# Optimization experiments

Hardware: AMD Instinct MI355X
Metric: run time of the kernel (lower is better)

Reference implementation:

```python
import jax, jax.numpy as jnp
import numpy as np

SR = 16000.0
WIN = 400
SHIFT = 160
NMEL = 80
PREEMPH = 0.97
EPS = float(np.finfo(np.float64).eps)


def _mel_banks(num_bins, win, sr):
    # kaldi-compatible triangular mel banks, low_freq=20, high_freq=nyquist
    def hz2mel(f):
        return 1127.0 * np.log(1.0 + f / 700.0)
    mlow, mhigh = hz2mel(20.0), hz2mel(sr / 2.0)
    d = (mhigh - mlow) / (num_bins + 1)
    left = mlow + np.arange(num_bins) * d
    center = left + d
    right = left + 2 * d
    fft_freqs = (sr / win) * np.arange(win // 2)
    mel = hz2mel(fft_freqs)[None, :]
    up = (mel - left[:, None]) / d
    down = (right[:, None] - mel) / d
    banks = np.maximum(0.0, np.minimum(up, down))
    banks = np.concatenate([banks, np.zeros((num_bins, 1))], axis=1)  # pad last rfft bin
    return jnp.asarray(banks, jnp.float32)

_BANKS = _mel_banks(NMEL, WIN, SR)
_WINDOW = jnp.asarray(0.5 - 0.5 * np.cos(2 * np.pi * np.arange(WIN) / (WIN - 1)), jnp.float32)


def setup_inputs() -> dict:
    key = jax.random.key(0)
    k1, k2 = jax.random.split(key)
    B, L = 64, 240000
    x = jax.random.normal(k1, (B, L), dtype=jnp.float32)
    T = jax.random.randint(k2, (B,), 1, L, dtype=jnp.int32)
    normalizer = jnp.full((NMEL,), 0.1, dtype=jnp.float32)  # Parameter init 1/10
    return {"x": x, "T": T, "normalizer": normalizer}


def _fbank(x, normalizer):
    B, L = x.shape
    n_frames = 1 + (L - WIN) // SHIFT  # snip_edges=True
    idx = np.arange(n_frames)[:, None] * SHIFT + np.arange(WIN)[None, :]
    frames = x[:, idx]
    # preemphasis: frame[i] -= 0.97 * frame[i-1]; first sample uses itself
    prev = jnp.concatenate([frames[..., :1], frames[..., :-1]], axis=-1)
    frames = (frames - PREEMPH * prev) * _WINDOW
    spec = jnp.abs(jnp.fft.rfft(frames, axis=-1)) ** 2
    mel = jnp.einsum('bfk,mk->bfm', spec, _BANKS)
    mel = jnp.log(jnp.maximum(mel, EPS))
    return mel * normalizer[None, None, :]


def reference(x, T, normalizer):
    fb = _fbank(x, normalizer)                            # (B, F, M)
    B, F, M = fb.shape
    # faithful to source: downsample_factor = max(T) / fbanks[0].shape[1] (= num_mel_bins)
    ds = jnp.max(T).astype(jnp.float32) / M
    T_ = (T.astype(jnp.float32) / ds).astype(jnp.int32)   # int() truncation, T >= 0
    mask = (jnp.arange(F)[None, :] < T_[:, None])[..., None]  # (B, F, 1)
    cnt = jnp.maximum(T_, 1).astype(fb.dtype)[:, None, None]
    mean = jnp.sum(jnp.where(mask, fb, 0.0), axis=1, keepdims=True) / cnt
    return jnp.where(mask, fb - mean, fb)
```

## Files before the change

kernel.cpp:

```cpp
#include <hip/hip_runtime.h>
#include <hip/hip_bf16.h>

#define BATCH   64
#define LSIG    240000
#define WIN     400
#define SHIFT   160
#define NFR     1498
#define NMEL    80
#define NBIN    200
#define NF      8
#define MAXW    14
#define SPECW   (NBIN + MAXW)

__device__ float g_win[WIN];
__device__ float g_tw1[11][20][2];
__device__ float g_tw2T[20][NBIN][2];
__device__ int   g_melStart[NMEL];
__device__ float g_melW[NMEL][MAXW];

__global__ void init_tables_kernel() {
    const int tid = threadIdx.x;
    const double PI = 3.14159265358979323846;
    __shared__ double melf[NBIN];
    __shared__ float root[WIN][2];

    for (int j = tid; j < WIN; j += 256) {
        double th = -2.0 * PI * (double)j / 400.0;
        root[j][0] = (float)cos(th);
        root[j][1] = (float)sin(th);
        g_win[j] = (float)(0.5 - 0.5 * cos(2.0 * PI * (double)j / 399.0));
    }
    for (int k = tid; k < NBIN; k += 256)
        melf[k] = 1127.0 * log(1.0 + (40.0 * (double)k) / 700.0);
    __syncthreads();

    for (int i = tid; i < 11 * 20; i += 256) {
        int r = i / 20, t1 = i % 20;
        int j = (20 * r * t1) % 400;
        g_tw1[r][t1][0] = root[j][0];
        g_tw1[r][t1][1] = root[j][1];
    }
    for (int i = tid; i < NBIN * 20; i += 256) {
        int t2 = i / NBIN, k = i - t2 * NBIN;
        int j = (k * t2) % 400;
        g_tw2T[t2][k][0] = root[j][0];
        g_tw2T[t2][k][1] = root[j][1];
    }
    if (tid < NMEL) {
        int m = tid;
        double mlow  = 1127.0 * log(1.0 + 20.0   / 700.0);
        double mhigh = 1127.0 * log(1.0 + 8000.0 / 700.0);
        double d     = (mhigh - mlow) / (double)(NMEL + 1);
        double inv_d = 1.0 / d;
        double left  = mlow + (double)m * d;
        double right = left + 2.0 * d;
        for (int j = 0; j < MAXW; j++) g_melW[m][j] = 0.0f;
        int start = 0; bool found = false;
        for (int k = 0; k < NBIN; k++) {
            double up = (melf[k] - left) * inv_d, down = (right - melf[k]) * inv_d;
            double w = fmax(0.0, fmin(up, down));
            if (w > 0.0) {
                if (!found) { start = k; found = true; }
                int j = k - start;
                if (j < MAXW) g_melW[m][j] = (float)w;
            }
        }
        g_melStart[m] = start;
    }
}

__global__ __launch_bounds__(256, 6)
void fbank_kernel(const float* __restrict__ x, const float* __restrict__ norm,
                  float* __restrict__ out) {
    const int ft = blockIdx.x;
    const int b  = blockIdx.y;
    const int f0 = ft * NF;
    const int nf = min(NF, NFR - f0);

    __shared__ __align__(16) float smem[3520 + NF * SPECW];
    float* Sb   = smem;
    float* xseg = smem + 3520;
    float* spec = smem + 3520;

    const float* xb = x + (size_t)b * LSIG + (size_t)f0 * SHIFT;
    const int seglen = (nf - 1) * SHIFT + WIN;
    for (int i = threadIdx.x; i < seglen; i += 256) xseg[i] = xb[i];
    __syncthreads();

    {
        const int p = threadIdx.x;
        if (p < nf * 20) {
            const int f = p / 20, t2 = p - f * 20;
            const float* xf = xseg + f * SHIFT;
            float yr[20];
#pragma unroll
            for (int t1 = 0; t1 < 20; t1++) {
                int t = t2 + 20 * t1;
                float xc = xf[t];
                float xp = xf[t > 0 ? t - 1 : 0];
                yr[t1] = (xc - 0.97f * xp) * g_win[t];
            }
#pragma unroll
            for (int r = 0; r <= 10; r++) {
                float ar = 0.0f, ai = 0.0f;
#pragma unroll
                for (int t1 = 0; t1 < 20; t1++) {
                    float c = g_tw1[r][t1][0], s = g_tw1[r][t1][1];
                    ar = fmaf(yr[t1], c, ar);
                    ai = fmaf(yr[t1], s, ai);
                }
                *(float2*)(Sb + ((f * 20 + t2) * 11 + r) * 2) = make_float2(ar, ai);
            }
        }
    }
    __syncthreads();

    {
        const int k = threadIdx.x;
        if (k < NBIN) {
            int r = k % 20;
            int rp  = (r > 10) ? 20 - r : r;
            float sg = (r > 10) ? -1.0f : 1.0f;
            float xr[NF], xi[NF];
#pragma unroll
            for (int f = 0; f < NF; f++) { xr[f] = 0.0f; xi[f] = 0.0f; }
            const float2* twp = (const float2*)&g_tw2T[0][k][0];
            for (int t2 = 0; t2 < 20; t2++) {
                float2 tw = twp[t2 * NBIN];
                float c = tw.x, s = tw.y * sg;
#pragma unroll
                for (int f = 0; f < NF; f++) {
                    float2 v = *(const float2*)(Sb + ((f * 20 + t2) * 11 + rp) * 2);
                    xr[f] = fmaf(c, v.x, fmaf(-s, v.y, xr[f]));
                    xi[f] = fmaf(s, v.x, fmaf(c,  v.y, xi[f]));
                }
            }
            for (int f = 0; f < nf; f++)
                spec[f * SPECW + k] = fmaf(xr[f], xr[f], xi[f] * xi[f]);
        } else if (k < NBIN + MAXW) {
            for (int f = 0; f < nf; f++) spec[f * SPECW + k] = 0.0f;
        }
    }
    __syncthreads();

    const int outs = nf * NMEL;
    for (int o = threadIdx.x; o < outs; o += 256) {
        int f = o / NMEL, m = o - f * NMEL;
        int ks = g_melStart[m];
        const float* sp = spec + f * SPECW + ks;
        float acc = 0.0f;
#pragma unroll
        for (int j = 0; j < MAXW; j++)
            acc = fmaf(g_melW[m][j], sp[j], acc);
        float mel = fmaxf(acc, 2.2204460492503131e-16f);
        float v = logf(mel) * norm[m];
        out[((size_t)b * NFR + (f0 + f)) * NMEL + m] = v;
    }
}

__global__ __launch_bounds__(256)
void meansub_kernel(float* __restrict__ out, const int* __restrict__ T) {
    const int b = blockIdx.x;
    __shared__ float part[3][NMEL];
    __shared__ float meanSh[NMEL];

    int maxT = T[0];
    for (int i = 1; i < BATCH; i++) maxT = max(maxT, T[i]);
    float ds = (float)maxT / (float)NMEL;
    int tb = (int)((float)T[b] / ds);

    const int q = threadIdx.x / NMEL;
    const int m = threadIdx.x - q * NMEL;
    float* pb = out + (size_t)b * NFR * NMEL;

    if (q < 3) {
        float s = 0.0f;
        for (int f = q; f < tb; f += 3) s += pb[(size_t)f * NMEL + m];
        part[q][m] = s;
    }
    __syncthreads();
    if (threadIdx.x < NMEL)
        meanSh[m] = (part[0][m] + part[1][m] + part[2][m]) / (float)max(tb, 1);
    __syncthreads();
    if (q < 3) {
        float mean = meanSh[m];
        for (int f = q; f < tb; f += 3) pb[(size_t)f * NMEL + m] -= mean;
    }
}

extern "C" void kernel_launch(void* const* d_in, const int* in_sizes, int n_in,
                              void* d_out, int out_size, void* d_ws, size_t ws_size,
                              hipStream_t stream) {
    const float* x    = (const float*)d_in[0];
    const int*   T    = (const int*)d_in[1];
    const float* norm = (const float*)d_in[2];
    float* out = (float*)d_out;

    init_tables_kernel<<<1, 256, 0, stream>>>();

    dim3 grid((NFR + NF - 1) / NF, BATCH);
    fbank_kernel<<<grid, 256, 0, stream>>>(x, norm, out);

    meansub_kernel<<<BATCH, 256, 0, stream>>>(out, T);
}
```

Baseline: 232.5 us.

## Compute twiddles, window and mel weights in-kernel, dropping the table init launch

```diff
diff --git a/kernel.cpp b/kernel.cpp
--- a/kernel.cpp
+++ b/kernel.cpp
@@ -12,62 +12,14 @@
 #define MAXW    14
 #define SPECW   (NBIN + MAXW)
 
-__device__ float g_win[WIN];
-__device__ float g_tw1[11][20][2];
-__device__ float g_tw2T[20][NBIN][2];
-__device__ int   g_melStart[NMEL];
-__device__ float g_melW[NMEL][MAXW];
-
-__global__ void init_tables_kernel() {
-    const int tid = threadIdx.x;
-    const double PI = 3.14159265358979323846;
-    __shared__ double melf[NBIN];
-    __shared__ float root[WIN][2];
-
-    for (int j = tid; j < WIN; j += 256) {
-        double th = -2.0 * PI * (double)j / 400.0;
-        root[j][0] = (float)cos(th);
-        root[j][1] = (float)sin(th);
-        g_win[j] = (float)(0.5 - 0.5 * cos(2.0 * PI * (double)j / 399.0));
-    }
-    for (int k = tid; k < NBIN; k += 256)
-        melf[k] = 1127.0 * log(1.0 + (40.0 * (double)k) / 700.0);
-    __syncthreads();
-
-    for (int i = tid; i < 11 * 20; i += 256) {
-        int r = i / 20, t1 = i % 20;
-        int j = (20 * r * t1) % 400;
-        g_tw1[r][t1][0] = root[j][0];
-        g_tw1[r][t1][1] = root[j][1];
-    }
-    for (int i = tid; i < NBIN * 20; i += 256) {
-        int t2 = i / NBIN, k = i - t2 * NBIN;
-        int j = (k * t2) % 400;
-        g_tw2T[t2][k][0] = root[j][0];
-        g_tw2T[t2][k][1] = root[j][1];
-    }
-    if (tid < NMEL) {
-        int m = tid;
-        double mlow  = 1127.0 * log(1.0 + 20.0   / 700.0);
-        double mhigh = 1127.0 * log(1.0 + 8000.0 / 700.0);
-        double d     = (mhigh - mlow) / (double)(NMEL + 1);
-        double inv_d = 1.0 / d;
-        double left  = mlow + (double)m * d;
-        double right = left + 2.0 * d;
-        for (int j = 0; j < MAXW; j++) g_melW[m][j] = 0.0f;
-        int start = 0; bool found = false;
-        for (int k = 0; k < NBIN; k++) {
-            double up = (melf[k] - left) * inv_d, down = (right - melf[k]) * inv_d;
-            double w = fmax(0.0, fmin(up, down));
-            if (w > 0.0) {
-                if (!found) { start = k; found = true; }
-                int j = k - start;
-                if (j < MAXW) g_melW[m][j] = (float)w;
-            }
-        }
-        g_melStart[m] = start;
-    }
-}
+#define SSTR    44
+#define SFR     (11 * SSTR)
+#define S_TOT   (NF * SFR)
+#define WIN_OFF  S_TOT
+#define TW1_OFF (S_TOT + 400)
+#define XSEG_OFF (S_TOT + 840)
+#define SPEC_OFF S_TOT
+#define LDS_TOT (S_TOT + 840 + 1520)
 
 __global__ __launch_bounds__(256, 6)
 void fbank_kernel(const float* __restrict__ x, const float* __restrict__ norm,
@@ -76,85 +28,125 @@
     const int b  = blockIdx.y;
     const int f0 = ft * NF;
     const int nf = min(NF, NFR - f0);
+    const int tid = threadIdx.x;
 
-    __shared__ __align__(16) float smem[3520 + NF * SPECW];
+    __shared__ __align__(16) float smem[LDS_TOT];
     float* Sb   = smem;
-    float* xseg = smem + 3520;
-    float* spec = smem + 3520;
+    float* winS = smem + WIN_OFF;
+    float* tw1S = smem + TW1_OFF;
+    float* xseg = smem + XSEG_OFF;
+    float* spec = smem + SPEC_OFF;
+
+    const float TWO_PI = 6.2831853071795864769f;
 
     const float* xb = x + (size_t)b * LSIG + (size_t)f0 * SHIFT;
     const int seglen = (nf - 1) * SHIFT + WIN;
-    for (int i = threadIdx.x; i < seglen; i += 256) xseg[i] = xb[i];
+    for (int i = tid; i < seglen; i += 256) xseg[i] = xb[i];
+
+    for (int j = tid; j < WIN; j += 256)
+        winS[j] = 0.5f - 0.5f * __cosf(TWO_PI * (float)j / 399.0f);
+    for (int i = tid; i < 220; i += 256) {
+        int r = i / 20, t1 = i - r * 20;
+        int j = (r * t1 * 20) % 400;
+        float th = (float)j * (-TWO_PI / 400.0f);
+        tw1S[2 * i]     = __cosf(th);
+        tw1S[2 * i + 1] = __sinf(th);
+    }
     __syncthreads();
 
-    {
-        const int p = threadIdx.x;
-        if (p < nf * 20) {
-            const int f = p / 20, t2 = p - f * 20;
-            const float* xf = xseg + f * SHIFT;
-            float yr[20];
+    if (tid < nf * 20) {
+        const int f = tid / 20, t2 = tid - f * 20;
+        const float* xf = xseg + f * SHIFT;
+        float yr[20];
+#pragma unroll
+        for (int t1 = 0; t1 < 20; t1++) {
+            int t = t2 + 20 * t1;
+            float xc = xf[t];
+            float xp = xf[t > 0 ? t - 1 : 0];
+            yr[t1] = (xc - 0.97f * xp) * winS[t];
+        }
+        float* Sf = Sb + f * SFR + t2 * 2;
+#pragma unroll
+        for (int r = 0; r <= 10; r++) {
+            float ar = 0.0f, ai = 0.0f;
 #pragma unroll
             for (int t1 = 0; t1 < 20; t1++) {
-                int t = t2 + 20 * t1;
-                float xc = xf[t];
-                float xp = xf[t > 0 ? t - 1 : 0];
-                yr[t1] = (xc - 0.97f * xp) * g_win[t];
+                float2 cs = *(const float2*)(tw1S + 2 * (r * 20 + t1));
+                ar = fmaf(yr[t1], cs.x, ar);
+                ai = fmaf(yr[t1], cs.y, ai);
             }
-#pragma unroll
-            for (int r = 0; r <= 10; r++) {
-                float ar = 0.0f, ai = 0.0f;
-#pragma unroll
-                for (int t1 = 0; t1 < 20; t1++) {
-                    float c = g_tw1[r][t1][0], s = g_tw1[r][t1][1];
-                    ar = fmaf(yr[t1], c, ar);
-                    ai = fmaf(yr[t1], s, ai);
-                }
-                *(float2*)(Sb + ((f * 20 + t2) * 11 + r) * 2) = make_float2(ar, ai);
-            }
+            *(float2*)(Sf + r * SSTR) = make_float2(ar, ai);
         }
     }
     __syncthreads();
 
     {
-        const int k = threadIdx.x;
+        const int k = tid;
         if (k < NBIN) {
             int r = k % 20;
-            int rp  = (r > 10) ? 20 - r : r;
+            int rp   = (r > 10) ? 20 - r : r;
             float sg = (r > 10) ? -1.0f : 1.0f;
-            float xr[NF], xi[NF];
+            float twc[20], tws[20];
 #pragma unroll
-            for (int f = 0; f < NF; f++) { xr[f] = 0.0f; xi[f] = 0.0f; }
-            const float2* twp = (const float2*)&g_tw2T[0][k][0];
             for (int t2 = 0; t2 < 20; t2++) {
-                float2 tw = twp[t2 * NBIN];
-                float c = tw.x, s = tw.y * sg;
+                int j = (k * t2) % 400;
+                float th = (float)j * (-TWO_PI / 400.0f);
+                twc[t2] = __cosf(th);
+                tws[t2] = __sinf(th) * sg;
+            }
+            for (int f = 0; f < nf; f++) {
+                const float4* Sf = (const float4*)(Sb + f * SFR + rp * SSTR);
+                float xr0 = 0.f, xi0 = 0.f, xr1 = 0.f, xi1 = 0.f;
 #pragma unroll
-                for (int f = 0; f < NF; f++) {
-                    float2 v = *(const float2*)(Sb + ((f * 20 + t2) * 11 + rp) * 2);
-                    xr[f] = fmaf(c, v.x, fmaf(-s, v.y, xr[f]));
-                    xi[f] = fmaf(s, v.x, fmaf(c,  v.y, xi[f]));
+                for (int q = 0; q < 10; q++) {
+                    float4 v = Sf[q];
+                    float c0 = twc[2 * q],     s0 = tws[2 * q];
+                    float c1 = twc[2 * q + 1], s1 = tws[2 * q + 1];
+                    xr0 = fmaf(c0, v.x, fmaf(-s0, v.y, xr0));
+                    xi0 = fmaf(s0, v.x, fmaf(c0,  v.y, xi0));
+                    xr1 = fmaf(c1, v.z, fmaf(-s1, v.w, xr1));
+                    xi1 = fmaf(s1, v.z, fmaf(c1,  v.w, xi1));
                 }
+                float xr = xr0 + xr1, xi = xi0 + xi1;
+                spec[f * SPECW + k] = fmaf(xr, xr, xi * xi);
             }
-            for (int f = 0; f < nf; f++)
-                spec[f * SPECW + k] = fmaf(xr[f], xr[f], xi[f] * xi[f]);
-        } else if (k < NBIN + MAXW) {
-            for (int f = 0; f < nf; f++) spec[f * SPECW + k] = 0.0f;
+        } else if (k < SPECW) {
+            for (int f = 0; f < NF; f++) spec[f * SPECW + k] = 0.0f;
         }
     }
     __syncthreads();
 
-    const int outs = nf * NMEL;
-    for (int o = threadIdx.x; o < outs; o += 256) {
-        int f = o / NMEL, m = o - f * NMEL;
-        int ks = g_melStart[m];
-        const float* sp = spec + f * SPECW + ks;
-        float acc = 0.0f;
+    if (tid < 240) {
+        const int m = tid % 80;
+        const int g = tid / 80;
+        const float mlow  = 1127.0f * __logf(1.0f + 20.0f / 700.0f);
+        const float mhigh = 1127.0f * __logf(1.0f + 8000.0f / 700.0f);
+        const float d     = (mhigh - mlow) * (1.0f / 81.0f);
+        const float left  = mlow + (float)m * d;
+        const float inv_d = 1.0f / d;
+        float freq_left = 700.0f * (__expf(left * (1.0f / 1127.0f)) - 1.0f);
+        int kstart = (int)floorf(freq_left * 0.025f) + 1;
+        float w[MAXW];
 #pragma unroll
-        for (int j = 0; j < MAXW; j++)
-            acc = fmaf(g_melW[m][j], sp[j], acc);
-        float mel = fmaxf(acc, 2.2204460492503131e-16f);
-        float v = logf(mel) * norm[m];
-        out[((size_t)b * NFR + (f0 + f)) * NMEL + m] = v;
+        for (int j = 0; j < MAXW; j++) {
+            float melk = 1127.0f * __logf(1.0f + (float)(kstart + j) * (40.0f / 700.0f));
+            float up = (melk - left) * inv_d;
+            float dn = 2.0f - up;
+            w[j] = fmaxf(0.0f, fminf(up, dn));
+        }
+        const float nm = norm[m];
+        for (int i = 0; i < 3; i++) {
+            int f = g + 3 * i;
+            if (f < nf) {
+                const float* sp = spec + f * SPECW + kstart;
+                float acc = 0.0f;
+#pragma unroll
+                for (int j = 0; j < MAXW; j++)
+                    acc = fmaf(w[j], sp[j], acc);
+                float mel = fmaxf(acc, 2.2204460492503131e-16f);
+                out[((size_t)b * NFR + (f0 + f)) * NMEL + m] = __logf(mel) * nm;
+            }
+        }
     }
 }
 
@@ -196,8 +188,6 @@
     const float* norm = (const float*)d_in[2];
     float* out = (float*)d_out;
 
-    init_tables_kernel<<<1, 256, 0, stream>>>();
-
     dim3 grid((NFR + NF - 1) / NF, BATCH);
     fbank_kernel<<<grid, 256, 0, stream>>>(x, norm, out);
 
```

Result: no change. 230.9 us (-0.7%).
